# Kernel tuning notes

Measured on AMD Instinct MI355X. Metric: run time of the kernel, lower is better.

The kernel has to match this reference:

```python
import jax, jax.numpy as jnp
import numpy as np

B, S, E, H = 8, 2048, 512, 8
D = E // H  # head_dim = 64


def setup_inputs() -> dict:
    key0 = jax.random.key(0)
    ks = jax.random.split(key0, 12)
    scale = 1.0 / np.sqrt(E)
    return {
        "value": jax.random.normal(ks[0], (B, S, E), jnp.float32),
        "key": jax.random.normal(ks[1], (B, S, E), jnp.float32),
        "query": jax.random.normal(ks[2], (B, S, E), jnp.float32),
        "mask": jax.random.randint(ks[3], (B, 1, 1, S), 0, 2, jnp.int32),
        "wq": jax.random.normal(ks[4], (E, E), jnp.float32) * scale,
        "bq": jnp.zeros((E,), jnp.float32),
        "wk": jax.random.normal(ks[5], (E, E), jnp.float32) * scale,
        "bk": jnp.zeros((E,), jnp.float32),
        "wv": jax.random.normal(ks[6], (E, E), jnp.float32) * scale,
        "bv": jnp.zeros((E,), jnp.float32),
        "wo": jax.random.normal(ks[7], (E, E), jnp.float32) * scale,
        "bo": jnp.zeros((E,), jnp.float32),
    }


def reference(value, key, query, mask, wq, bq, wk, bk, wv, bv, wo, bo):
    b, s, e = query.shape
    # projections
    q = (query @ wq + bq).reshape(b, s, H, D)  # (B,S,H,D)
    k = (key @ wk + bk).reshape(b, s, H, D)
    v = (value @ wv + bv).reshape(b, s, H, D)
    # scaled dot-product logits: (B,H,Sq,Sk)
    logits = jnp.einsum("bqhd,bkhd->bhqk", q, k) / jnp.sqrt(jnp.asarray(D, q.dtype))
    logits = logits + mask.astype(logits.dtype) * -1e9  # mask==1 -> blocked
    attn = jax.nn.softmax(logits, axis=-1)
    out = jnp.einsum("bhqk,bkhd->bqhd", attn, v).reshape(b, s, e)
    return out @ wo + bo
```

## Files before the change

kernel.cpp:

```cpp
#include <hip/hip_runtime.h>

#define Bz 8
#define Sz 2048
#define Ez 512
#define Hz 8
#define Dz 64

typedef _Float16 f16;
typedef __attribute__((ext_vector_type(2))) _Float16 f16x2;
typedef __attribute__((ext_vector_type(8))) _Float16 f16x8;
typedef __attribute__((ext_vector_type(4))) float f32x4;

#define LOG2E 1.44269504f

__device__ __forceinline__ void async16(const void* g, void* l) {
    __builtin_amdgcn_global_load_lds(
        (const __attribute__((address_space(1))) unsigned int*)g,
        (__attribute__((address_space(3))) unsigned int*)l, 16, 0, 0);
}

__device__ __forceinline__ f16x2 pkrtz(float a, float b) {
    return __builtin_bit_cast(f16x2, __builtin_amdgcn_cvt_pkrtz(a, b));
}

__device__ __forceinline__ int swz(int row) {
    return (row & 7) ^ ((2 * ((row >> 3) & 3)) & 7);
}

__global__ __launch_bounds__(256)
void prep_kernel(const float* __restrict__ W0, const float* __restrict__ W1,
                 const float* __restrict__ W2, const float* __restrict__ W3,
                 f16* __restrict__ T0, f16* __restrict__ T1,
                 f16* __restrict__ T2, f16* __restrict__ T3,
                 const int* __restrict__ mask, int* __restrict__ idx,
                 int* __restrict__ slen, f16* __restrict__ vt)
{
    const int blk = blockIdx.x;
    const int tid = threadIdx.x;
    if (blk < 256) {
        __shared__ float S[64][68];
        const int z = blk >> 6, rest = blk & 63;
        const float* W = (z==0)?W0:(z==1)?W1:(z==2)?W2:W3;
        f16*         T = (z==0)?T0:(z==1)?T1:(z==2)?T2:T3;
        const float sc = (z == 0) ? 0.125f * LOG2E : 1.0f;
        const int k0 = (rest & 7) * 64, n0 = (rest >> 3) * 64;
        {
            int kr = tid >> 4, nc = (tid & 15) * 4;
            #pragma unroll
            for (int i = 0; i < 4; ++i) {
                float4 w4 = *(const float4*)&W[(size_t)(k0 + kr + i*16) * Ez + n0 + nc];
                S[kr + i*16][nc+0] = w4.x; S[kr + i*16][nc+1] = w4.y;
                S[kr + i*16][nc+2] = w4.z; S[kr + i*16][nc+3] = w4.w;
            }
        }
        __syncthreads();
        {
            int n = tid >> 2, kq = tid & 3;
            f16 h[16];
            #pragma unroll
            for (int j = 0; j < 16; ++j) h[j] = (f16)(S[kq*16 + j][n] * sc);
            f16* dst = &T[(size_t)(n0 + n) * Ez + k0 + kq*16];
            *(uint4*)&dst[0] = *(uint4*)&h[0];
            *(uint4*)&dst[8] = *(uint4*)&h[8];
        }
        return;
    }
    const int b = blk - 256;
    if (b >= Bz) return;
    __shared__ int sc2[2][256];
    __shared__ int ssl;
    const int* mp = mask + (size_t)b * Sz;
    int m[8], c = 0;
    #pragma unroll
    for (int j = 0; j < 8; ++j) { m[j] = mp[tid*8 + j]; c += (m[j] == 0); }
    sc2[0][tid] = c;
    __syncthreads();
    int src = 0;
    #pragma unroll
    for (int s = 1; s < 256; s <<= 1) {
        int vv = sc2[src][tid] + ((tid >= s) ? sc2[src][tid - s] : 0);
        sc2[src ^ 1][tid] = vv;
        src ^= 1;
        __syncthreads();
    }
    int incl = sc2[src][tid];
    int base = incl - c;
    if (tid == 255) { slen[b] = incl; ssl = incl; }
    int kk = base;
    #pragma unroll
    for (int j = 0; j < 8; ++j)
        if (m[j] == 0) idx[(size_t)b * Sz + (kk++)] = tid*8 + j;
    __syncthreads();
    const int sl2 = ssl;
    const int pad = (sl2 + 63) & ~63;
    if (pad > sl2) {
        for (int pr = tid; pr < Hz * Dz; pr += 256) {
            f16* dst = vt + ((size_t)b * Hz * Dz + pr) * Sz;
            for (int j = sl2; j < pad; ++j) dst[j] = (f16)0.f;
        }
    }
}

__global__ __launch_bounds__(256)
void cast_kernel(const float* __restrict__ q, const float* __restrict__ key,
                 const float* __restrict__ value, const int* __restrict__ idx,
                 const int* __restrict__ slen,
                 f16* __restrict__ qa, f16* __restrict__ ka, f16* __restrict__ va)
{
    const int blk = blockIdx.x;
    const int tid = threadIdx.x;
    if (blk < 4096) {
        const size_t off = ((size_t)blk * 256 + tid) * 8;
        float4 x0 = *(const float4*)&q[off];
        float4 x1 = *(const float4*)&q[off + 4];
        f16 h[8];
        f16x2 p0 = pkrtz(x0.x, x0.y), p1 = pkrtz(x0.z, x0.w);
        f16x2 p2 = pkrtz(x1.x, x1.y), p3 = pkrtz(x1.z, x1.w);
        h[0] = p0[0]; h[1] = p0[1]; h[2] = p1[0]; h[3] = p1[1];
        h[4] = p2[0]; h[5] = p2[1]; h[6] = p3[0]; h[7] = p3[1];
        *(uint4*)&qa[off] = *(uint4*)h;
        return;
    }
    const int r = blk - 4096;
    const int zt = r >> 12;
    const int rem = r & 4095;
    const int b = rem >> 9, grp = rem & 511;
    const int sl = slen[b];
    if (grp * 4 >= sl) return;
    const int w = tid >> 6, lane = tid & 63;
    const int j = grp * 4 + w;
    if (j >= sl) return;
    const int s = idx[(size_t)b * Sz + j];
    const float* srcp = ((zt == 0) ? key : value) + ((size_t)b * Sz + s) * Ez + lane * 8;
    f16* dst = ((zt == 0) ? ka : va) + ((size_t)b * Sz + j) * Ez + lane * 8;
    float4 x0 = *(const float4*)&srcp[0];
    float4 x1 = *(const float4*)&srcp[4];
    f16 h[8];
    f16x2 p0 = pkrtz(x0.x, x0.y), p1 = pkrtz(x0.z, x0.w);
    f16x2 p2 = pkrtz(x1.x, x1.y), p3 = pkrtz(x1.z, x1.w);
    h[0] = p0[0]; h[1] = p0[1]; h[2] = p1[0]; h[3] = p1[1];
    h[4] = p2[0]; h[5] = p2[1]; h[6] = p3[0]; h[7] = p3[1];
    *(uint4*)&dst[lane * 0] = *(uint4*)h;
}

__global__ __launch_bounds__(256, 4)
void proj_gemm(const f16* __restrict__ qa, const f16* __restrict__ ka,
               const f16* __restrict__ va,
               const f16* __restrict__ wtq, const f16* __restrict__ wtk,
               const f16* __restrict__ wtv,
               const float* __restrict__ bqp, const float* __restrict__ bkp,
               const float* __restrict__ bvp, const int* __restrict__ slen,
               f16* __restrict__ qp, f16* __restrict__ kp, f16* __restrict__ vt)
{
    __shared__ __align__(16) char lds[32768];
    const int z = blockIdx.z;
    const int m0 = blockIdx.x * 128, n0 = blockIdx.y * 128;
    const int bb = m0 >> 11;
    const int m0c = m0 & (Sz - 1);

    int sl = Sz;
    if (z != 0) {
        sl = slen[bb];
        if (m0c >= sl) return;
    }

    const f16* A  = (z==0)?qa:(z==1)?ka:va;
    const f16* Wt = (z==0)?wtq:(z==1)?wtk:wtv;
    const float* bias = (z==0)?bqp:(z==1)?bkp:bvp;
    const float bscale = (z==0) ? 0.125f*LOG2E : 1.0f;

    const int tid  = threadIdx.x;
    const int lane = tid & 63, w = tid >> 6;
    const int col  = lane & 15, quad = lane >> 4;
    const int wm = w & 1, wn = w >> 1;
    const int srow = lane >> 2, schunk = lane & 3;

    f32x4 acc[4][4];
    #pragma unroll
    for (int i = 0; i < 4; ++i)
        #pragma unroll
        for (int j = 0; j < 4; ++j) acc[i][j] = (f32x4){0.f,0.f,0.f,0.f};

    auto issue = [&](int t, int buf) {
        f16* As = (f16*)(lds + buf * 16384);
        f16* Ws = As + 4096;
        #pragma unroll
        for (int i = 0; i < 2; ++i) {
            const int row = w*32 + i*16 + srow;
            const int cl = schunk ^ ((row >> 1) & 3);
            async16(&A[(size_t)(m0 + row) * Ez + t*32 + cl*8],  &As[row*32 + schunk*8]);
            async16(&Wt[(size_t)(n0 + row) * Ez + t*32 + cl*8], &Ws[row*32 + schunk*8]);
        }
    };

    issue(0, 0);
    const int xrc = (col >> 1) & 3;

    for (int t = 0; t < 16; ++t) {
        const int cur = t & 1;
        __syncthreads();
        if (t < 15) issue(t + 1, cur ^ 1);
        f16* As = (f16*)(lds + cur * 16384);
        f16* Ws = As + 4096;
        f16x8 af[4];
        #pragma unroll
        for (int mi = 0; mi < 4; ++mi)
            af[mi] = *(const f16x8*)&As[(wm*64 + mi*16 + col)*32 + ((quad ^ xrc)*8)];
        #pragma unroll
        for (int ni = 0; ni < 4; ++ni) {
            f16x8 wf = *(const f16x8*)&Ws[(wn*64 + ni*16 + col)*32 + ((quad ^ xrc)*8)];
            #pragma unroll
            for (int mi = 0; mi < 4; ++mi)
                acc[mi][ni] = __builtin_amdgcn_mfma_f32_16x16x32_f16(af[mi], wf, acc[mi][ni], 0,0,0);
        }
    }

    const int rw = tid >> 1, half = tid & 1;

    f16* Tr  = (f16*)lds;
    f16* Tr2 = (f16*)lds;
    #pragma unroll
    for (int p = 0; p < 2; ++p) {
        __syncthreads();
        if (wn == p) {
            #pragma unroll
            for (int ni = 0; ni < 4; ++ni) {
                float bv = bias[n0 + p*64 + ni*16 + col] * bscale;
                #pragma unroll
                for (int mi = 0; mi < 4; ++mi)
                    #pragma unroll
                    for (int rr = 0; rr < 4; ++rr) {
                        const int ml = wm*64 + mi*16 + quad*4 + rr;
                        const float val = acc[mi][ni][rr] + bv;
                        if (z != 2) Tr[ml*72 + ni*16 + col] = (f16)val;
                        else        Tr2[(ni*16 + col)*136 + ml] = (f16)val;
                    }
            }
        }
        __syncthreads();
        const int hh = (n0 >> 6) + p;
        if (z != 2) {
            const int rank = m0c + rw;
            if (z == 0 || rank < sl) {
                f16* C16 = (z == 0) ? qp : kp;
                f16* dst = &C16[(((size_t)bb*Hz + hh)*Sz + rank)*Dz + half*32];
                const f16* srcp = &Tr[rw*72 + half*32];
                #pragma unroll
                for (int j = 0; j < 4; ++j)
                    *(uint4*)&dst[j*8] = *(const uint4*)&srcp[j*8];
            }
        } else {
            const int d = tid >> 2, mq = tid & 3;
            const int base = m0c + mq*32;
            if (base < sl) {
                f16* dstb = vt + (((size_t)bb*Hz + hh)*Dz + d)*Sz + base;
                const f16* srcr = &Tr2[d*136 + mq*32];
                int lim = sl - base; if (lim > 32) lim = 32;
                if (lim == 32) {
                    #pragma unroll
                    for (int g = 0; g < 4; ++g)
                        *(uint4*)&dstb[g*8] = *(const uint4*)&srcr[g*8];
                } else {
                    const int full = lim >> 3;
                    for (int g = 0; g < full; ++g)
                        *(uint4*)&dstb[g*8] = *(const uint4*)&srcr[g*8];
                    for (int e = full*8; e < lim; ++e) dstb[e] = srcr[e];
                }
            }
        }
    }
}

__global__ __launch_bounds__(256, 4)
void out_gemm(const f16* __restrict__ A, const f16* __restrict__ Wt,
              const float* __restrict__ bias, float* __restrict__ Cf)
{
    __shared__ __align__(16) char lds[32768];
    const int tid  = threadIdx.x;
    const int lane = tid & 63, w = tid >> 6;
    const int col  = lane & 15, quad = lane >> 4;
    const int wm = w & 1, wn = w >> 1;
    const int m0 = blockIdx.x * 128, n0 = blockIdx.y * 128;
    const int srow = lane >> 2, schunk = lane & 3;

    f32x4 acc[4][4];
    #pragma unroll
    for (int i = 0; i < 4; ++i)
        #pragma unroll
        for (int j = 0; j < 4; ++j) acc[i][j] = (f32x4){0.f,0.f,0.f,0.f};

    auto issue = [&](int t, int buf) {
        f16* As = (f16*)(lds + buf * 16384);
        f16* Ws = As + 4096;
        #pragma unroll
        for (int i = 0; i < 2; ++i) {
            int row = w*32 + i*16 + srow;
            int cl = schunk ^ ((row >> 1) & 3);
            async16(&A[(size_t)(m0 + row) * Ez + t*32 + cl*8],  &As[row*32 + schunk*8]);
            async16(&Wt[(size_t)(n0 + row) * Ez + t*32 + cl*8], &Ws[row*32 + schunk*8]);
        }
    };

    issue(0, 0);
    const int xrc = (col >> 1) & 3;

    for (int t = 0; t < 16; ++t) {
        const int cur = t & 1;
        __syncthreads();
        if (t < 15) issue(t + 1, cur ^ 1);
        f16* As = (f16*)(lds + cur * 16384);
        f16* Ws = As + 4096;
        f16x8 af[4];
        #pragma unroll
        for (int mi = 0; mi < 4; ++mi)
            af[mi] = *(const f16x8*)&As[(wm*64 + mi*16 + col)*32 + ((quad ^ xrc)*8)];
        #pragma unroll
        for (int ni = 0; ni < 4; ++ni) {
            f16x8 wf = *(const f16x8*)&Ws[(wn*64 + ni*16 + col)*32 + ((quad ^ xrc)*8)];
            #pragma unroll
            for (int mi = 0; mi < 4; ++mi)
                acc[mi][ni] = __builtin_amdgcn_mfma_f32_16x16x32_f16(af[mi], wf, acc[mi][ni], 0,0,0);
        }
    }

    #pragma unroll
    for (int ni = 0; ni < 4; ++ni) {
        int n = n0 + wn*64 + ni*16 + col;
        float bv = bias[n];
        #pragma unroll
        for (int mi = 0; mi < 4; ++mi)
            #pragma unroll
            for (int rr = 0; rr < 4; ++rr) {
                int m = m0 + wm*64 + mi*16 + quad*4 + rr;
                Cf[(size_t)m * Ez + n] = acc[mi][ni][rr] + bv;
            }
    }
}

__global__ __launch_bounds__(256, 4)
void attn_f16(const f16* __restrict__ Q, const f16* __restrict__ K,
              const f16* __restrict__ VT, const int* __restrict__ slen,
              f16* __restrict__ O)
{
    __shared__ __align__(16) f16 KS[2][64*64];
    __shared__ __align__(16) f16 VS[2][64*64];

    const int tid  = threadIdx.x;
    const int lane = tid & 63, w = tid >> 6;
    const int col  = lane & 15, quad = lane >> 4;

    const int blk = blockIdx.x;
    const int xcd = blk & 7, slot = blk >> 3;
    const int bh = xcd + 8 * (slot >> 4);
    const int qb = slot & 15;
    const int b = bh >> 3, h = bh & 7;

    const int sl = slen[b];
    int nt = (sl + 63) >> 6;
    if (nt < 1) nt = 1;

    const int q0 = qb * 128 + w * 32;

    f16x8 qf[2][2];
    #pragma unroll
    for (int qt = 0; qt < 2; ++qt)
        #pragma unroll
        for (int ks = 0; ks < 2; ++ks)
            qf[qt][ks] = *(const f16x8*)&Q[((size_t)bh*Sz + q0 + qt*16 + col)*Dz + ks*32 + quad*8];

    const f16* Kp = K + (size_t)bh * Sz * Dz;
    const f16* Vp = VT + (size_t)bh * Dz * Sz;

    const int srow = lane >> 3, sch = lane & 7;
    const int row0 = w*16 + srow, row1 = row0 + 8;
    const int cl0 = sch ^ swz(row0), cl1 = sch ^ swz(row1);

    int keyrow[4], gk[4];
    #pragma unroll
    for (int kc = 0; kc < 4; ++kc) {
        keyrow[kc] = 32*(kc>>1) + 8*(col>>2) + 4*(kc&1) + (col&3);
        gk[kc] = swz(keyrow[kc]);
    }

    f32x4 oacc[2][4];
    #pragma unroll
    for (int qt = 0; qt < 2; ++qt)
        #pragma unroll
        for (int dc = 0; dc < 4; ++dc) oacc[qt][dc] = (f32x4){0.f,0.f,0.f,0.f};
    const f32x4 zero4 = (f32x4){0.f, 0.f, 0.f, 0.f};
    f32x4 lacc[2] = {(f32x4){0.f,0.f,0.f,0.f}, (f32x4){0.f,0.f,0.f,0.f}};
    f16x8 one8;
    #pragma unroll
    for (int i = 0; i < 8; ++i) one8[i] = (f16)1.0f;

    auto issue = [&](int t, int buf) {
        async16(&Kp[(size_t)(t*64 + row0)*Dz + cl0*8], &KS[buf][row0*64 + sch*8]);
        async16(&Vp[(size_t)row0*Sz + t*64 + cl0*8],   &VS[buf][row0*64 + sch*8]);
        async16(&Kp[(size_t)(t*64 + row1)*Dz + cl1*8], &KS[buf][row1*64 + sch*8]);
        async16(&Vp[(size_t)row1*Sz + t*64 + cl1*8],   &VS[buf][row1*64 + sch*8]);
    };

    issue(0, 0);

    for (int t = 0; t < nt; ++t) {
        const int cur = t & 1;
        __syncthreads();
        if (t + 1 < nt) issue(t + 1, cur ^ 1);

        f32x4 sc[2][4];
        __builtin_amdgcn_s_setprio(1);
        #pragma unroll
        for (int kc = 0; kc < 4; ++kc) {
            f16x8 kf0 = *(const f16x8*)&KS[cur][keyrow[kc]*64 + ((quad ^ gk[kc])*8)];
            f16x8 kf1 = *(const f16x8*)&KS[cur][keyrow[kc]*64 + (((4 + quad) ^ gk[kc])*8)];
            sc[0][kc] = __builtin_amdgcn_mfma_f32_16x16x32_f16(kf0, qf[0][0], zero4, 0,0,0);
            sc[1][kc] = __builtin_amdgcn_mfma_f32_16x16x32_f16(kf0, qf[1][0], zero4, 0,0,0);
            sc[0][kc] = __builtin_amdgcn_mfma_f32_16x16x32_f16(kf1, qf[0][1], sc[0][kc], 0,0,0);
            sc[1][kc] = __builtin_amdgcn_mfma_f32_16x16x32_f16(kf1, qf[1][1], sc[1][kc], 0,0,0);
        }
        __builtin_amdgcn_s_setprio(0);

        const bool last = (t == nt - 1);
        union { f16x2 h2[4]; f16x8 h8; } ph[2][2];
        #pragma unroll
        for (int qt = 0; qt < 2; ++qt) {
            #pragma unroll
            for (int kg = 0; kg < 2; ++kg) {
                float e0 = __builtin_amdgcn_exp2f(sc[qt][2*kg][0]);
                float e1 = __builtin_amdgcn_exp2f(sc[qt][2*kg][1]);
                float e2 = __builtin_amdgcn_exp2f(sc[qt][2*kg][2]);
                float e3 = __builtin_amdgcn_exp2f(sc[qt][2*kg][3]);
                float e4 = __builtin_amdgcn_exp2f(sc[qt][2*kg+1][0]);
                float e5 = __builtin_amdgcn_exp2f(sc[qt][2*kg+1][1]);
                float e6 = __builtin_amdgcn_exp2f(sc[qt][2*kg+1][2]);
                float e7 = __builtin_amdgcn_exp2f(sc[qt][2*kg+1][3]);
                if (last) {
                    int rem = sl - t*64 - 32*kg - 8*quad;
                    e0 = (rem > 0) ? e0 : 0.f; e1 = (rem > 1) ? e1 : 0.f;
                    e2 = (rem > 2) ? e2 : 0.f; e3 = (rem > 3) ? e3 : 0.f;
                    e4 = (rem > 4) ? e4 : 0.f; e5 = (rem > 5) ? e5 : 0.f;
                    e6 = (rem > 6) ? e6 : 0.f; e7 = (rem > 7) ? e7 : 0.f;
                }
                ph[qt][kg].h2[0] = pkrtz(e0, e1);
                ph[qt][kg].h2[1] = pkrtz(e2, e3);
                ph[qt][kg].h2[2] = pkrtz(e4, e5);
                ph[qt][kg].h2[3] = pkrtz(e6, e7);
            }
        }

        __builtin_amdgcn_s_setprio(1);
        lacc[0] = __builtin_amdgcn_mfma_f32_16x16x32_f16(one8, ph[0][0].h8, lacc[0], 0,0,0);
        lacc[1] = __builtin_amdgcn_mfma_f32_16x16x32_f16(one8, ph[1][0].h8, lacc[1], 0,0,0);
        lacc[0] = __builtin_amdgcn_mfma_f32_16x16x32_f16(one8, ph[0][1].h8, lacc[0], 0,0,0);
        lacc[1] = __builtin_amdgcn_mfma_f32_16x16x32_f16(one8, ph[1][1].h8, lacc[1], 0,0,0);
        #pragma unroll
        for (int dc = 0; dc < 4; ++dc) {
            const int d = dc*16 + col;
            const int gd = swz(d);
            #pragma unroll
            for (int kg = 0; kg < 2; ++kg) {
                f16x8 vf = *(const f16x8*)&VS[cur][d*64 + (((kg*4 + quad) ^ gd)*8)];
                oacc[0][dc] = __builtin_amdgcn_mfma_f32_16x16x32_f16(vf, ph[0][kg].h8, oacc[0][dc], 0,0,0);
                oacc[1][dc] = __builtin_amdgcn_mfma_f32_16x16x32_f16(vf, ph[1][kg].h8, oacc[1][dc], 0,0,0);
            }
        }
        __builtin_amdgcn_s_setprio(0);
    }

    float inv[2];
    inv[0] = 1.0f / lacc[0][0];
    inv[1] = 1.0f / lacc[1][0];
    #pragma unroll
    for (int qt = 0; qt < 2; ++qt) {
        const int q = q0 + qt*16 + col;
        f16* op = &O[((size_t)b*Sz + q)*Ez + h*Dz];
        #pragma unroll
        for (int dc = 0; dc < 4; ++dc) {
            f16 ov[4] = {(f16)(oacc[qt][dc][0]*inv[qt]), (f16)(oacc[qt][dc][1]*inv[qt]),
                         (f16)(oacc[qt][dc][2]*inv[qt]), (f16)(oacc[qt][dc][3]*inv[qt])};
            *(uint2*)&op[dc*16 + quad*4] = *(uint2*)ov;
        }
    }
}

extern "C" void kernel_launch(void* const* d_in, const int* in_sizes, int n_in,
                              void* d_out, int out_size, void* d_ws, size_t ws_size,
                              hipStream_t stream)
{
    const float* value = (const float*)d_in[0];
    const float* key   = (const float*)d_in[1];
    const float* query = (const float*)d_in[2];
    const int*   mask  = (const int*)d_in[3];
    const float* wq = (const float*)d_in[4];
    const float* bq = (const float*)d_in[5];
    const float* wk = (const float*)d_in[6];
    const float* bk = (const float*)d_in[7];
    const float* wv = (const float*)d_in[8];
    const float* bv = (const float*)d_in[9];
    const float* wo = (const float*)d_in[10];
    const float* bo = (const float*)d_in[11];
    float* out = (float*)d_out;

    const size_t nW   = (size_t)Ez * Ez;
    const size_t nAct = (size_t)Bz * Sz * Ez;
    f16* wtq = (f16*)d_ws;
    f16* wtk = wtq + nW;
    f16* wtv = wtk + nW;
    f16* wto = wtv + nW;
    f16* qa  = wto + nW;
    f16* ka  = qa + nAct;
    f16* va  = ka + nAct;
    f16* qp  = va + nAct;
    f16* kp  = qp + nAct;
    f16* vt  = kp + nAct;
    f16* o16 = vt + nAct;
    int* idxp = (int*)(o16 + nAct);
    int* slenp = idxp + Bz * Sz;

    prep_kernel<<<264, 256, 0, stream>>>(wq, wk, wv, wo, wtq, wtk, wtv, wto,
                                         mask, idxp, slenp, vt);

    cast_kernel<<<12288, 256, 0, stream>>>(query, key, value, idxp, slenp,
                                           qa, ka, va);

    proj_gemm<<<dim3(128, 4, 3), 256, 0, stream>>>(qa, ka, va, wtq, wtk, wtv,
                                                   bq, bk, bv, slenp,
                                                   qp, kp, vt);

    attn_f16<<<1024, 256, 0, stream>>>(qp, kp, vt, slenp, o16);

    out_gemm<<<dim3(128, 4), 256, 0, stream>>>(o16, wto, bo, out);
}
```

Measured before the change: 275.7 us.

## Fuse fp32-to-fp16 cast and mask gather into projection GEMM A-tile loads

Removes the separate cast kernel and its fp16 staging buffers. The projection GEMM now reads fp32 query/key/value directly, gathers unmasked key/value rows through the index list, and converts to fp16 in registers before writing into swizzled LDS. The A-tile load for the next step is issued before the MFMA loop and written to LDS after it, so global latency overlaps with compute. In exchange, each GEMM block reads fp32 A tiles (twice the bytes of fp16) for every N tile, so A is re-read four times across blockIdx.y. Register pressure also rises from holding the prefetched float4 values.

```diff
diff --git a/kernel.cpp b/kernel.cpp
--- a/kernel.cpp
+++ b/kernel.cpp
@@ -101,55 +101,14 @@
     }
 }
 
-__global__ __launch_bounds__(256)
-void cast_kernel(const float* __restrict__ q, const float* __restrict__ key,
-                 const float* __restrict__ value, const int* __restrict__ idx,
-                 const int* __restrict__ slen,
-                 f16* __restrict__ qa, f16* __restrict__ ka, f16* __restrict__ va)
-{
-    const int blk = blockIdx.x;
-    const int tid = threadIdx.x;
-    if (blk < 4096) {
-        const size_t off = ((size_t)blk * 256 + tid) * 8;
-        float4 x0 = *(const float4*)&q[off];
-        float4 x1 = *(const float4*)&q[off + 4];
-        f16 h[8];
-        f16x2 p0 = pkrtz(x0.x, x0.y), p1 = pkrtz(x0.z, x0.w);
-        f16x2 p2 = pkrtz(x1.x, x1.y), p3 = pkrtz(x1.z, x1.w);
-        h[0] = p0[0]; h[1] = p0[1]; h[2] = p1[0]; h[3] = p1[1];
-        h[4] = p2[0]; h[5] = p2[1]; h[6] = p3[0]; h[7] = p3[1];
-        *(uint4*)&qa[off] = *(uint4*)h;
-        return;
-    }
-    const int r = blk - 4096;
-    const int zt = r >> 12;
-    const int rem = r & 4095;
-    const int b = rem >> 9, grp = rem & 511;
-    const int sl = slen[b];
-    if (grp * 4 >= sl) return;
-    const int w = tid >> 6, lane = tid & 63;
-    const int j = grp * 4 + w;
-    if (j >= sl) return;
-    const int s = idx[(size_t)b * Sz + j];
-    const float* srcp = ((zt == 0) ? key : value) + ((size_t)b * Sz + s) * Ez + lane * 8;
-    f16* dst = ((zt == 0) ? ka : va) + ((size_t)b * Sz + j) * Ez + lane * 8;
-    float4 x0 = *(const float4*)&srcp[0];
-    float4 x1 = *(const float4*)&srcp[4];
-    f16 h[8];
-    f16x2 p0 = pkrtz(x0.x, x0.y), p1 = pkrtz(x0.z, x0.w);
-    f16x2 p2 = pkrtz(x1.x, x1.y), p3 = pkrtz(x1.z, x1.w);
-    h[0] = p0[0]; h[1] = p0[1]; h[2] = p1[0]; h[3] = p1[1];
-    h[4] = p2[0]; h[5] = p2[1]; h[6] = p3[0]; h[7] = p3[1];
-    *(uint4*)&dst[lane * 0] = *(uint4*)h;
-}
-
 __global__ __launch_bounds__(256, 4)
-void proj_gemm(const f16* __restrict__ qa, const f16* __restrict__ ka,
-               const f16* __restrict__ va,
+void proj_gemm(const float* __restrict__ Aq, const float* __restrict__ Ak,
+               const float* __restrict__ Av,
                const f16* __restrict__ wtq, const f16* __restrict__ wtk,
                const f16* __restrict__ wtv,
                const float* __restrict__ bqp, const float* __restrict__ bkp,
-               const float* __restrict__ bvp, const int* __restrict__ slen,
+               const float* __restrict__ bvp, const int* __restrict__ idx,
+               const int* __restrict__ slen,
                f16* __restrict__ qp, f16* __restrict__ kp, f16* __restrict__ vt)
 {
     __shared__ __align__(16) char lds[32768];
@@ -164,7 +123,7 @@
         if (m0c >= sl) return;
     }
 
-    const f16* A  = (z==0)?qa:(z==1)?ka:va;
+    const float* Af = (z==0)?Aq:(z==1)?Ak:Av;
     const f16* Wt = (z==0)?wtq:(z==1)?wtk:wtv;
     const float* bias = (z==0)?bqp:(z==1)?bkp:bvp;
     const float bscale = (z==0) ? 0.125f*LOG2E : 1.0f;
@@ -174,6 +133,20 @@
     const int col  = lane & 15, quad = lane >> 4;
     const int wm = w & 1, wn = w >> 1;
     const int srow = lane >> 2, schunk = lane & 3;
+    const int awp = schunk ^ ((srow >> 1) & 3);
+
+    size_t arow[2];
+    #pragma unroll
+    for (int i = 0; i < 2; ++i) {
+        const int row = w*32 + i*16 + srow;
+        if (z == 0) {
+            arow[i] = (size_t)(m0 + row) * Ez;
+        } else {
+            const int j = m0c + row;
+            const int jc = (j < sl) ? j : sl - 1;
+            arow[i] = ((size_t)bb * Sz + idx[(size_t)bb * Sz + jc]) * Ez;
+        }
+    }
 
     f32x4 acc[4][4];
     #pragma unroll
@@ -181,25 +154,46 @@
         #pragma unroll
         for (int j = 0; j < 4; ++j) acc[i][j] = (f32x4){0.f,0.f,0.f,0.f};
 
-    auto issue = [&](int t, int buf) {
+    float4 ar[2][2];
+    auto loadA = [&](int t) {
+        #pragma unroll
+        for (int i = 0; i < 2; ++i) {
+            const float* p = &Af[arow[i] + t*32 + schunk*8];
+            ar[i][0] = *(const float4*)&p[0];
+            ar[i][1] = *(const float4*)&p[4];
+        }
+    };
+    auto writeA = [&](int buf) {
         f16* As = (f16*)(lds + buf * 16384);
-        f16* Ws = As + 4096;
+        #pragma unroll
+        for (int i = 0; i < 2; ++i) {
+            f16 h[8];
+            f16x2 p0 = pkrtz(ar[i][0].x, ar[i][0].y), p1 = pkrtz(ar[i][0].z, ar[i][0].w);
+            f16x2 p2 = pkrtz(ar[i][1].x, ar[i][1].y), p3 = pkrtz(ar[i][1].z, ar[i][1].w);
+            h[0] = p0[0]; h[1] = p0[1]; h[2] = p1[0]; h[3] = p1[1];
+            h[4] = p2[0]; h[5] = p2[1]; h[6] = p3[0]; h[7] = p3[1];
+            *(uint4*)&As[(w*32 + i*16 + srow)*32 + awp*8] = *(uint4*)h;
+        }
+    };
+    auto issueW = [&](int t, int buf) {
+        f16* Ws = (f16*)(lds + buf * 16384) + 4096;
         #pragma unroll
         for (int i = 0; i < 2; ++i) {
             const int row = w*32 + i*16 + srow;
             const int cl = schunk ^ ((row >> 1) & 3);
-            async16(&A[(size_t)(m0 + row) * Ez + t*32 + cl*8],  &As[row*32 + schunk*8]);
             async16(&Wt[(size_t)(n0 + row) * Ez + t*32 + cl*8], &Ws[row*32 + schunk*8]);
         }
     };
 
-    issue(0, 0);
+    loadA(0);
+    issueW(0, 0);
+    writeA(0);
     const int xrc = (col >> 1) & 3;
 
     for (int t = 0; t < 16; ++t) {
         const int cur = t & 1;
         __syncthreads();
-        if (t < 15) issue(t + 1, cur ^ 1);
+        if (t < 15) { issueW(t + 1, cur ^ 1); loadA(t + 1); }
         f16* As = (f16*)(lds + cur * 16384);
         f16* Ws = As + 4096;
         f16x8 af[4];
@@ -213,6 +207,7 @@
             for (int mi = 0; mi < 4; ++mi)
                 acc[mi][ni] = __builtin_amdgcn_mfma_f32_16x16x32_f16(af[mi], wf, acc[mi][ni], 0,0,0);
         }
+        if (t < 15) writeA(cur ^ 1);
     }
 
     const int rw = tid >> 1, half = tid & 1;
@@ -507,10 +502,7 @@
     f16* wtk = wtq + nW;
     f16* wtv = wtk + nW;
     f16* wto = wtv + nW;
-    f16* qa  = wto + nW;
-    f16* ka  = qa + nAct;
-    f16* va  = ka + nAct;
-    f16* qp  = va + nAct;
+    f16* qp  = wto + nW;
     f16* kp  = qp + nAct;
     f16* vt  = kp + nAct;
     f16* o16 = vt + nAct;
@@ -520,11 +512,9 @@
     prep_kernel<<<264, 256, 0, stream>>>(wq, wk, wv, wo, wtq, wtk, wtv, wto,
                                          mask, idxp, slenp, vt);
 
-    cast_kernel<<<12288, 256, 0, stream>>>(query, key, value, idxp, slenp,
-                                           qa, ka, va);
-
-    proj_gemm<<<dim3(128, 4, 3), 256, 0, stream>>>(qa, ka, va, wtq, wtk, wtv,
-                                                   bq, bk, bv, slenp,
+    proj_gemm<<<dim3(128, 4, 3), 256, 0, stream>>>(query, key, value,
+                                                   wtq, wtk, wtv,
+                                                   bq, bk, bv, idxp, slenp,
                                                    qp, kp, vt);
 
     attn_f16<<<1024, 256, 0, stream>>>(qp, kp, vt, slenp, o16);
```

After: 274.4 us. No clear change (-0.5%).
